# Kernel optimization log

Measured on AMD Instinct MI355X. Metric: run time of the kernel, lower is better.

## Reference

```python
import jax, jax.numpy as jnp
import numpy as np

D_IN = 1024
D_OUT = 1024
N_HEADS = 16
HEAD_DIM = D_OUT // N_HEADS
B = 2
S = 2048


def setup_inputs() -> dict:
    key = jax.random.key(0)
    ks = jax.random.split(key, 6)
    scale = 0.02
    x = jax.random.normal(ks[0], (B, S, D_IN), dtype=jnp.float32)
    # torch nn.Linear stores weight as [out, in]; y = x @ W.T + b
    Wq = jax.random.normal(ks[1], (D_OUT, D_IN), dtype=jnp.float32) * scale
    Wk = jax.random.normal(ks[2], (D_OUT, D_IN), dtype=jnp.float32) * scale
    Wv = jax.random.normal(ks[3], (D_OUT, D_IN), dtype=jnp.float32) * scale
    Wo = jax.random.normal(ks[4], (D_OUT, D_OUT), dtype=jnp.float32) * scale
    bo = jax.random.normal(ks[5], (D_OUT,), dtype=jnp.float32) * scale
    return {"x": x, "Wq": Wq, "Wk": Wk, "Wv": Wv, "Wo": Wo, "bo": bo}


def reference(x, Wq, Wk, Wv, Wo, bo):
    b, n, _ = x.shape
    # projections (no qkv bias)
    q = jnp.einsum('bnd,ed->bne', x, Wq).reshape(b, n, N_HEADS, HEAD_DIM).transpose(0, 2, 1, 3)
    k = jnp.einsum('bnd,ed->bne', x, Wk).reshape(b, n, N_HEADS, HEAD_DIM).transpose(0, 2, 1, 3)
    v = jnp.einsum('bnd,ed->bne', x, Wv).reshape(b, n, N_HEADS, HEAD_DIM).transpose(0, 2, 1, 3)
    # scores [b, h, s, s]
    scores = jnp.einsum('bhqd,bhkd->bhqk', q, k) / jnp.sqrt(jnp.float32(HEAD_DIM))
    causal = jnp.tril(jnp.ones((n, n), dtype=bool))
    scores = jnp.where(causal, scores, -jnp.inf)
    attn = jax.nn.softmax(scores, axis=-1)  # dropout p=0 -> identity
    ctx = jnp.einsum('bhqk,bhkd->bhqd', attn, v)
    ctx = ctx.transpose(0, 2, 1, 3).reshape(b, n, D_OUT)
    out = jnp.einsum('bnd,ed->bne', ctx, Wo) + bo
    return out
```

## Files before the change

### kernel.cpp

```cpp
#include <hip/hip_runtime.h>

typedef unsigned short u16;
typedef unsigned int u32;
typedef short bf16x8 __attribute__((ext_vector_type(8)));
typedef short bf16x4 __attribute__((ext_vector_type(4)));
typedef float f32x4 __attribute__((ext_vector_type(4)));
typedef u32 u32x2 __attribute__((ext_vector_type(2)));

#define LOG2E 1.4426950408889634f
#define QSCALE (0.125f * LOG2E)

__device__ __forceinline__ u16 f2b(float f) {
  u32 u = __builtin_bit_cast(u32, f);
  u32 r = (u + 0x7FFFu + ((u >> 16) & 1u)) >> 16;
  return (u16)r;
}

__device__ __forceinline__ bf16x8 cvt8(const float* p) {
  const f32x4 a = *(const f32x4*)p;
  const f32x4 b = *(const f32x4*)(p + 4);
  bf16x8 r = { (short)f2b(a[0]), (short)f2b(a[1]), (short)f2b(a[2]),
               (short)f2b(a[3]), (short)f2b(b[0]), (short)f2b(b[1]),
               (short)f2b(b[2]), (short)f2b(b[3]) };
  return r;
}

__device__ __forceinline__ void gl_lds16(const u16* g, u16* l) {
  __builtin_amdgcn_global_load_lds(
      (const __attribute__((address_space(1))) u32*)(const void*)g,
      (__attribute__((address_space(3))) u32*)(void*)l, 16, 0, 0);
}

__global__ __launch_bounds__(256) void convert_qw_kernel(
    const float* __restrict__ x, const float* __restrict__ wq,
    const float* __restrict__ wk, const float* __restrict__ wv,
    u16* __restrict__ xb, u16* __restrict__ wb) {
  const int i = blockIdx.x * 256 + threadIdx.x;
  if (i >= 917504) return;
  const float* src;
  u16* dst;
  size_t off;
  if (i < 524288) {
    src = x; dst = xb; off = (size_t)i * 8;
  } else {
    const int j = i - 524288;
    const int mat = j >> 17, r = j & 131071;
    src = (mat == 0) ? wq : ((mat == 1) ? wk : wv);
    dst = wb + (size_t)mat * 1048576u;
    off = (size_t)r * 8;
  }
  *(bf16x8*)(dst + off) = cvt8(src + off);
}

__global__ __launch_bounds__(256) void convert_wo_kernel(
    const float* __restrict__ wo, u16* __restrict__ wob) {
  const int i = blockIdx.x * 256 + threadIdx.x;
  if (i >= 131072) return;
  const size_t off = (size_t)i * 8;
  *(bf16x8*)(wob + off) = cvt8(wo + off);
}

__device__ __forceinline__ void gemm_core2(const u16* A, const u16* W,
                                           int m0, int n0, int tid,
                                           u16* As, u16* Bs,
                                           f32x4 (&acc)[4][4]) {
  const int lane = tid & 63, wave = tid >> 6;
  const int wr = wave >> 1, wc = wave & 1;
  const int l15 = lane & 15, quad = lane >> 4;

  const int srow = wave * 16 + (lane >> 2);
  const int csrc =
      (((lane & 3) ^ ((lane >> 2) & 3) ^ ((lane >> 4) & 3)) << 3);
  const u16* ga = A + (size_t)(m0 + srow) * 1024 + csrc;
  const u16* gw = W + (size_t)(n0 + srow) * 1024 + csrc;
  u16* la = As + wave * 16 * 32;
  u16* lb = Bs + wave * 16 * 32;

  const int rswz = (l15 & 3) ^ ((l15 >> 2) & 3);
  const u16* ar = As + (wr * 64 + l15) * 32 + ((quad ^ rswz) << 3);
  const u16* br = Bs + (wc * 64 + l15) * 32 + ((quad ^ rswz) << 3);

  for (int k0 = 0; k0 < 1024; k0 += 32) {
    __syncthreads();
    gl_lds16(ga + k0, la);
    gl_lds16(ga + k0 + (size_t)64 * 1024, la + 64 * 32);
    gl_lds16(gw + k0, lb);
    gl_lds16(gw + k0 + (size_t)64 * 1024, lb + 64 * 32);
    __syncthreads();
    bf16x8 af[4], bfr[4];
#pragma unroll
    for (int i = 0; i < 4; ++i) af[i] = *(const bf16x8*)(ar + i * 16 * 32);
#pragma unroll
    for (int i = 0; i < 4; ++i) bfr[i] = *(const bf16x8*)(br + i * 16 * 32);
#pragma unroll
    for (int mt = 0; mt < 4; ++mt)
#pragma unroll
      for (int nt = 0; nt < 4; ++nt)
        acc[mt][nt] = __builtin_amdgcn_mfma_f32_16x16x32_bf16(
            af[mt], bfr[nt], acc[mt][nt], 0, 0, 0);
  }
}

__global__ __launch_bounds__(256, 3) void gemm_qkv_kernel(
    const u16* __restrict__ xb, const u16* __restrict__ wb,
    u16* __restrict__ qo, u16* __restrict__ ko, u16* __restrict__ vt) {
  __shared__ __align__(16) u16 As[128 * 32];
  __shared__ __align__(16) u16 Bs[128 * 32];
  const int tid = threadIdx.x;
  const int m0 = blockIdx.x * 128;
  const int mat = blockIdx.y >> 3;
  const int n0 = (blockIdx.y & 7) * 128;
  const u16* W = wb + (size_t)mat * 1048576u;

  f32x4 acc[4][4] = {};
  gemm_core2(xb, W, m0, n0, tid, As, Bs, acc);

  const int lane = tid & 63, wave = tid >> 6;
  const int wr = wave >> 1, wc = wave & 1;
  const int l15 = lane & 15, quad = lane >> 4;

  if (mat < 2) {
    u16* out = (mat == 0) ? qo : ko;
    const float sc = (mat == 0) ? QSCALE : 1.0f;
#pragma unroll
    for (int mt = 0; mt < 4; ++mt) {
      const int gr = m0 + wr * 64 + mt * 16 + quad * 4;
#pragma unroll
      for (int nt = 0; nt < 4; ++nt) {
        const int gc = n0 + wc * 64 + nt * 16 + l15;
#pragma unroll
        for (int r = 0; r < 4; ++r)
          out[(size_t)(gr + r) * 1024 + gc] = f2b(acc[mt][nt][r] * sc);
      }
    }
  } else {
#pragma unroll
    for (int mt = 0; mt < 4; ++mt) {
      const int gr = m0 + wr * 64 + mt * 16 + quad * 4;
      const int b = gr >> 11;
      const int s = gr & 2047;
#pragma unroll
      for (int nt = 0; nt < 4; ++nt) {
        const int gc = n0 + wc * 64 + nt * 16 + l15;
        bf16x4 pk = { (short)f2b(acc[mt][nt][0]), (short)f2b(acc[mt][nt][1]),
                      (short)f2b(acc[mt][nt][2]), (short)f2b(acc[mt][nt][3]) };
        *(bf16x4*)&vt[(size_t)(b * 1024 + gc) * 2048 + s] = pk;
      }
    }
  }
}

__global__ __launch_bounds__(256, 3) void gemm_out_kernel(
    const u16* __restrict__ ctx, const u16* __restrict__ wob,
    const float* __restrict__ bo, float* __restrict__ out) {
  __shared__ __align__(16) u16 As[128 * 32];
  __shared__ __align__(16) u16 Bs[128 * 32];
  const int tid = threadIdx.x;
  const int m0 = blockIdx.x * 128;
  const int n0 = blockIdx.y * 128;

  f32x4 acc[4][4] = {};
  gemm_core2(ctx, wob, m0, n0, tid, As, Bs, acc);

  const int lane = tid & 63, wave = tid >> 6;
  const int wr = wave >> 1, wc = wave & 1;
  const int l15 = lane & 15, quad = lane >> 4;
#pragma unroll
  for (int nt = 0; nt < 4; ++nt) {
    const int gc = n0 + wc * 64 + nt * 16 + l15;
    const float bv = bo[gc];
#pragma unroll
    for (int mt = 0; mt < 4; ++mt) {
      const int gr = m0 + wr * 64 + mt * 16 + quad * 4;
#pragma unroll
      for (int r = 0; r < 4; ++r)
        out[(size_t)(gr + r) * 1024 + gc] = acc[mt][nt][r] + bv;
    }
  }
}

__global__ __launch_bounds__(256, 4) void flash_kernel(
    const u16* q, const u16* __restrict__ k,
    const u16* __restrict__ vt, u16* ctx) {
  __shared__ __align__(16) u16 Ks[2][4096];
  __shared__ __align__(16) u16 Vs[2][4096];
  __shared__ __align__(16) u16 plds_all[4][1024];

  const int tid = threadIdx.x;
  const int wave = tid >> 6, lane = tid & 63;
  const int l15 = lane & 15, quad = lane >> 4;

  const int g = blockIdx.x;
  const int xcd = g & 7;
  const int s = g >> 3;
  const int bh_local = s >> 5;
  const int c = s & 31;
  const int qv = (bh_local & 1) ? (31 - c) : c;
  const int q0b = qv * 64;
  const int ntiles = qv + 1;
  const int bh = xcd + 8 * bh_local;
  const int b = bh >> 4, h = bh & 15;
  const int m = q0b + wave * 16 + l15;

  const u16* qrow = q + ((size_t)(b * 2048 + m) * 1024 + h * 64);
  const bf16x8 qf0 = *(const bf16x8*)(qrow + quad * 8);
  const bf16x8 qf1 = *(const bf16x8*)(qrow + 32 + quad * 8);

  const int sr = wave * 16 + (lane >> 3);
  const int csrc = (((lane & 7) ^ ((lane >> 3) & 7)) << 3);
  const u16* kg = k + (size_t)(b * 2048) * 1024 + h * 64;
  const u16* vg = vt + (size_t)(b * 1024 + h * 64) * 2048;
  u16* plds = plds_all[wave];
  const int swz = (l15 & 7);

  f32x4 o[4] = {};
  float m_run = -INFINITY, l_lane = 0.0f;

#pragma unroll
  for (int i = 0; i < 2; ++i) {
    const int r = sr + i * 8;
    gl_lds16(kg + (size_t)r * 1024 + csrc, &Ks[0][wave * 1024 + i * 512]);
    gl_lds16(vg + (size_t)r * 2048 + csrc, &Vs[0][wave * 1024 + i * 512]);
  }
  __syncthreads();

  int buf = 0;
  for (int t = 0; t < ntiles; ++t) {
    const int n0 = t * 64;
    if (t + 1 < ntiles) {
      const int n1 = n0 + 64;
      const int nb = buf ^ 1;
#pragma unroll
      for (int i = 0; i < 2; ++i) {
        const int r = sr + i * 8;
        gl_lds16(kg + (size_t)(n1 + r) * 1024 + csrc,
                 &Ks[nb][wave * 1024 + i * 512]);
        gl_lds16(vg + (size_t)r * 2048 + n1 + csrc,
                 &Vs[nb][wave * 1024 + i * 512]);
      }
    }

    f32x4 st[4];
#pragma unroll
    for (int s4 = 0; s4 < 4; ++s4) {
      const u16* kr = &Ks[buf][(s4 * 16 + l15) * 64];
      const bf16x8 kf0 = *(const bf16x8*)(kr + ((quad ^ swz) << 3));
      const bf16x8 kf1 = *(const bf16x8*)(kr + (((4 | quad) ^ swz) << 3));
      f32x4 a = {};
      a = __builtin_amdgcn_mfma_f32_16x16x32_bf16(kf0, qf0, a, 0, 0, 0);
      a = __builtin_amdgcn_mfma_f32_16x16x32_bf16(kf1, qf1, a, 0, 0, 0);
      st[s4] = a;
    }

    float s[16];
#pragma unroll
    for (int s4 = 0; s4 < 4; ++s4)
#pragma unroll
      for (int r = 0; r < 4; ++r) s[s4 * 4 + r] = st[s4][r];
    if (t == ntiles - 1) {
#pragma unroll
      for (int s4 = 0; s4 < 4; ++s4)
#pragma unroll
        for (int r = 0; r < 4; ++r) {
          const int kv = n0 + s4 * 16 + quad * 4 + r;
          if (kv > m) s[s4 * 4 + r] = -INFINITY;
        }
    }
    float t8[8], t4[4];
#pragma unroll
    for (int i = 0; i < 8; ++i) t8[i] = fmaxf(s[i], s[i + 8]);
#pragma unroll
    for (int i = 0; i < 4; ++i) t4[i] = fmaxf(t8[i], t8[i + 4]);
    float mx = fmaxf(fmaxf(t4[0], t4[1]), fmaxf(t4[2], t4[3]));
    mx = fmaxf(mx, __shfl_xor(mx, 16));
    mx = fmaxf(mx, __shfl_xor(mx, 32));

    float mbase;
    if (__all(mx <= m_run + 8.0f)) {
      mbase = m_run;
    } else {
      mbase = fmaxf(m_run, mx);
      const float alpha = exp2f(m_run - mbase);
      l_lane *= alpha;
#pragma unroll
      for (int dt = 0; dt < 4; ++dt) o[dt] *= alpha;
      m_run = mbase;
    }

    float p[16];
#pragma unroll
    for (int i = 0; i < 16; ++i) p[i] = exp2f(s[i] - mbase);
    float u8[8], u4[4];
#pragma unroll
    for (int i = 0; i < 8; ++i) u8[i] = p[i] + p[i + 8];
#pragma unroll
    for (int i = 0; i < 4; ++i) u4[i] = u8[i] + u8[i + 4];
    l_lane += (u4[0] + u4[1]) + (u4[2] + u4[3]);

#pragma unroll
    for (int s4 = 0; s4 < 4; ++s4) {
      u32 c0, c1;
      asm("v_cvt_pk_bf16_f32 %0, %1, %2"
          : "=v"(c0) : "v"(p[s4 * 4 + 0]), "v"(p[s4 * 4 + 1]));
      asm("v_cvt_pk_bf16_f32 %0, %1, %2"
          : "=v"(c1) : "v"(p[s4 * 4 + 2]), "v"(p[s4 * 4 + 3]));
      const int wchunk = ((s4 * 2 + (quad >> 1)) ^ swz) << 3;
      u32x2 w = { c0, c1 };
      *(u32x2*)&plds[l15 * 64 + wchunk + ((quad & 1) << 2)] = w;
    }
    asm volatile("s_waitcnt lgkmcnt(0)" ::: "memory");

#pragma unroll
    for (int ks = 0; ks < 2; ++ks) {
      const bf16x8 pf =
          *(const bf16x8*)&plds[l15 * 64 + (((ks * 4 + quad) ^ swz) << 3)];
#pragma unroll
      for (int dt = 0; dt < 4; ++dt) {
        const u16* vr = &Vs[buf][(dt * 16 + l15) * 64];
        const bf16x8 vf =
            *(const bf16x8*)(vr + ((((ks << 2) | quad) ^ swz) << 3));
        o[dt] = __builtin_amdgcn_mfma_f32_16x16x32_bf16(vf, pf, o[dt], 0, 0, 0);
      }
    }

    __syncthreads();
    buf ^= 1;
  }

  float l = l_lane;
  l += __shfl_xor(l, 16);
  l += __shfl_xor(l, 32);
  const float inv = 1.0f / l;
  u16* crow = ctx + ((size_t)(b * 2048 + m) * 1024 + h * 64);
#pragma unroll
  for (int dt = 0; dt < 4; ++dt) {
    bf16x4 ov = { (short)f2b(o[dt][0] * inv), (short)f2b(o[dt][1] * inv),
                  (short)f2b(o[dt][2] * inv), (short)f2b(o[dt][3] * inv) };
    *(bf16x4*)&crow[dt * 16 + quad * 4] = ov;
  }
}

extern "C" void kernel_launch(void* const* d_in, const int* in_sizes, int n_in,
                              void* d_out, int out_size, void* d_ws,
                              size_t ws_size, hipStream_t stream) {
  const float* x  = (const float*)d_in[0];
  const float* wq = (const float*)d_in[1];
  const float* wk = (const float*)d_in[2];
  const float* wv = (const float*)d_in[3];
  const float* wo = (const float*)d_in[4];
  const float* bo = (const float*)d_in[5];
  float* out = (float*)d_out;

  u16* qb = (u16*)d_ws;
  u16* kb = qb + 4194304u;
  u16* vt = kb + 4194304u;
  u16* ctx = qb;

  u16* xb = (u16*)d_out;
  u16* wb = xb + 4194304u;
  u16* wob = kb;

  convert_qw_kernel<<<3584, 256, 0, stream>>>(x, wq, wk, wv, xb, wb);
  gemm_qkv_kernel<<<dim3(32, 24), 256, 0, stream>>>(xb, wb, qb, kb, vt);
  flash_kernel<<<1024, 256, 0, stream>>>(qb, kb, vt, ctx);
  convert_wo_kernel<<<512, 256, 0, stream>>>(wo, wob);
  gemm_out_kernel<<<dim3(32, 8), 256, 0, stream>>>(ctx, wob, bo, out);
}
```

Measured before the change: 191.7 us.

## Double-buffer GEMM LDS tiles and software-pipeline QK of next tile in flash attention

The shared GEMM core now double-buffers the A/B LDS tiles, issuing the next k-slice's global-to-LDS loads before computing on the current one, with one barrier per iteration instead of two. The flash kernel is restructured so the QK^T scores for tile t+1 are computed while the softmax and PV of tile t proceed. V fragments are preloaded into registers so the K/V buffer can be refilled for tile t+2 earlier. Flash launch bounds drop from 4 to 3 blocks per SM to make room for the extra live registers, trading occupancy for overlap.

```diff
diff --git a/kernel.cpp b/kernel.cpp
--- a/kernel.cpp
+++ b/kernel.cpp
@@ -60,7 +60,7 @@
   *(bf16x8*)(wob + off) = cvt8(wo + off);
 }
 
-__device__ __forceinline__ void gemm_core2(const u16* A, const u16* W,
+__device__ __forceinline__ void gemm_core3(const u16* A, const u16* W,
                                            int m0, int n0, int tid,
                                            u16* As, u16* Bs,
                                            f32x4 (&acc)[4][4]) {
@@ -73,20 +73,28 @@
       (((lane & 3) ^ ((lane >> 2) & 3) ^ ((lane >> 4) & 3)) << 3);
   const u16* ga = A + (size_t)(m0 + srow) * 1024 + csrc;
   const u16* gw = W + (size_t)(n0 + srow) * 1024 + csrc;
-  u16* la = As + wave * 16 * 32;
-  u16* lb = Bs + wave * 16 * 32;
+  const int lo = wave * 16 * 32;
 
   const int rswz = (l15 & 3) ^ ((l15 >> 2) & 3);
-  const u16* ar = As + (wr * 64 + l15) * 32 + ((quad ^ rswz) << 3);
-  const u16* br = Bs + (wc * 64 + l15) * 32 + ((quad ^ rswz) << 3);
-
-  for (int k0 = 0; k0 < 1024; k0 += 32) {
-    __syncthreads();
+  const int aoff = (wr * 64 + l15) * 32 + ((quad ^ rswz) << 3);
+  const int boff = (wc * 64 + l15) * 32 + ((quad ^ rswz) << 3);
+
+  auto stage = [&](int k0, int db) {
+    u16* la = As + db * 4096 + lo;
+    u16* lb = Bs + db * 4096 + lo;
     gl_lds16(ga + k0, la);
     gl_lds16(ga + k0 + (size_t)64 * 1024, la + 64 * 32);
     gl_lds16(gw + k0, lb);
     gl_lds16(gw + k0 + (size_t)64 * 1024, lb + 64 * 32);
-    __syncthreads();
+  };
+
+  stage(0, 0);
+  __syncthreads();
+  int db = 0;
+  for (int k0 = 0; k0 < 1024; k0 += 32) {
+    if (k0 + 32 < 1024) stage(k0 + 32, db ^ 1);
+    const u16* ar = As + db * 4096 + aoff;
+    const u16* br = Bs + db * 4096 + boff;
     bf16x8 af[4], bfr[4];
 #pragma unroll
     for (int i = 0; i < 4; ++i) af[i] = *(const bf16x8*)(ar + i * 16 * 32);
@@ -98,14 +106,16 @@
       for (int nt = 0; nt < 4; ++nt)
         acc[mt][nt] = __builtin_amdgcn_mfma_f32_16x16x32_bf16(
             af[mt], bfr[nt], acc[mt][nt], 0, 0, 0);
+    __syncthreads();
+    db ^= 1;
   }
 }
 
 __global__ __launch_bounds__(256, 3) void gemm_qkv_kernel(
     const u16* __restrict__ xb, const u16* __restrict__ wb,
     u16* __restrict__ qo, u16* __restrict__ ko, u16* __restrict__ vt) {
-  __shared__ __align__(16) u16 As[128 * 32];
-  __shared__ __align__(16) u16 Bs[128 * 32];
+  __shared__ __align__(16) u16 As[2 * 128 * 32];
+  __shared__ __align__(16) u16 Bs[2 * 128 * 32];
   const int tid = threadIdx.x;
   const int m0 = blockIdx.x * 128;
   const int mat = blockIdx.y >> 3;
@@ -113,7 +123,7 @@
   const u16* W = wb + (size_t)mat * 1048576u;
 
   f32x4 acc[4][4] = {};
-  gemm_core2(xb, W, m0, n0, tid, As, Bs, acc);
+  gemm_core3(xb, W, m0, n0, tid, As, Bs, acc);
 
   const int lane = tid & 63, wave = tid >> 6;
   const int wr = wave >> 1, wc = wave & 1;
@@ -153,14 +163,14 @@
 __global__ __launch_bounds__(256, 3) void gemm_out_kernel(
     const u16* __restrict__ ctx, const u16* __restrict__ wob,
     const float* __restrict__ bo, float* __restrict__ out) {
-  __shared__ __align__(16) u16 As[128 * 32];
-  __shared__ __align__(16) u16 Bs[128 * 32];
+  __shared__ __align__(16) u16 As[2 * 128 * 32];
+  __shared__ __align__(16) u16 Bs[2 * 128 * 32];
   const int tid = threadIdx.x;
   const int m0 = blockIdx.x * 128;
   const int n0 = blockIdx.y * 128;
 
   f32x4 acc[4][4] = {};
-  gemm_core2(ctx, wob, m0, n0, tid, As, Bs, acc);
+  gemm_core3(ctx, wob, m0, n0, tid, As, Bs, acc);
 
   const int lane = tid & 63, wave = tid >> 6;
   const int wr = wave >> 1, wc = wave & 1;
@@ -179,7 +189,7 @@
   }
 }
 
-__global__ __launch_bounds__(256, 4) void flash_kernel(
+__global__ __launch_bounds__(256, 3) void flash_kernel(
     const u16* q, const u16* __restrict__ k,
     const u16* __restrict__ vt, u16* ctx) {
   __shared__ __align__(16) u16 Ks[2][4096];
@@ -192,9 +202,9 @@
 
   const int g = blockIdx.x;
   const int xcd = g & 7;
-  const int s = g >> 3;
-  const int bh_local = s >> 5;
-  const int c = s & 31;
+  const int sidx = g >> 3;
+  const int bh_local = sidx >> 5;
+  const int c = sidx & 31;
   const int qv = (bh_local & 1) ? (31 - c) : c;
   const int q0b = qv * 64;
   const int ntiles = qv + 1;
@@ -213,44 +223,54 @@
   u16* plds = plds_all[wave];
   const int swz = (l15 & 7);
 
-  f32x4 o[4] = {};
-  float m_run = -INFINITY, l_lane = 0.0f;
-
-#pragma unroll
-  for (int i = 0; i < 2; ++i) {
-    const int r = sr + i * 8;
-    gl_lds16(kg + (size_t)r * 1024 + csrc, &Ks[0][wave * 1024 + i * 512]);
-    gl_lds16(vg + (size_t)r * 2048 + csrc, &Vs[0][wave * 1024 + i * 512]);
-  }
-  __syncthreads();
-
-  int buf = 0;
-  for (int t = 0; t < ntiles; ++t) {
-    const int n0 = t * 64;
-    if (t + 1 < ntiles) {
-      const int n1 = n0 + 64;
-      const int nb = buf ^ 1;
-#pragma unroll
-      for (int i = 0; i < 2; ++i) {
-        const int r = sr + i * 8;
-        gl_lds16(kg + (size_t)(n1 + r) * 1024 + csrc,
-                 &Ks[nb][wave * 1024 + i * 512]);
-        gl_lds16(vg + (size_t)r * 2048 + n1 + csrc,
-                 &Vs[nb][wave * 1024 + i * 512]);
-      }
-    }
-
-    f32x4 st[4];
+  auto stage = [&](int n, int db) {
+#pragma unroll
+    for (int i = 0; i < 2; ++i) {
+      const int r = sr + i * 8;
+      gl_lds16(kg + (size_t)(n * 64 + r) * 1024 + csrc,
+               &Ks[db][wave * 1024 + i * 512]);
+      gl_lds16(vg + (size_t)r * 2048 + n * 64 + csrc,
+               &Vs[db][wave * 1024 + i * 512]);
+    }
+  };
+  auto qk_tile = [&](int db, f32x4 (&dst)[4]) {
 #pragma unroll
     for (int s4 = 0; s4 < 4; ++s4) {
-      const u16* kr = &Ks[buf][(s4 * 16 + l15) * 64];
+      const u16* kr = &Ks[db][(s4 * 16 + l15) * 64];
       const bf16x8 kf0 = *(const bf16x8*)(kr + ((quad ^ swz) << 3));
       const bf16x8 kf1 = *(const bf16x8*)(kr + (((4 | quad) ^ swz) << 3));
       f32x4 a = {};
       a = __builtin_amdgcn_mfma_f32_16x16x32_bf16(kf0, qf0, a, 0, 0, 0);
       a = __builtin_amdgcn_mfma_f32_16x16x32_bf16(kf1, qf1, a, 0, 0, 0);
-      st[s4] = a;
-    }
+      dst[s4] = a;
+    }
+  };
+
+  f32x4 o[4] = {};
+  float m_run = -INFINITY, l_lane = 0.0f;
+
+  stage(0, 0);
+  __syncthreads();
+  f32x4 st[4];
+  qk_tile(0, st);
+  stage(1, 1);
+
+  int buf = 0;
+  for (int t = 0; t < ntiles; ++t) {
+    __syncthreads();
+
+    bf16x8 vf[8];
+#pragma unroll
+    for (int ks = 0; ks < 2; ++ks)
+#pragma unroll
+      for (int dt = 0; dt < 4; ++dt)
+        vf[ks * 4 + dt] = *(const bf16x8*)(&Vs[buf][(dt * 16 + l15) * 64] +
+                                           ((((ks << 2) | quad) ^ swz) << 3));
+    f32x4 stn[4];
+    if (t + 1 < ntiles) qk_tile(buf ^ 1, stn);
+
+    __syncthreads();
+    if (t + 2 < ntiles) stage(t + 2, buf);
 
     float s[16];
 #pragma unroll
@@ -258,6 +278,7 @@
 #pragma unroll
       for (int r = 0; r < 4; ++r) s[s4 * 4 + r] = st[s4][r];
     if (t == ntiles - 1) {
+      const int n0 = t * 64;
 #pragma unroll
       for (int s4 = 0; s4 < 4; ++s4)
 #pragma unroll
@@ -315,15 +336,15 @@
       const bf16x8 pf =
           *(const bf16x8*)&plds[l15 * 64 + (((ks * 4 + quad) ^ swz) << 3)];
 #pragma unroll
-      for (int dt = 0; dt < 4; ++dt) {
-        const u16* vr = &Vs[buf][(dt * 16 + l15) * 64];
-        const bf16x8 vf =
-            *(const bf16x8*)(vr + ((((ks << 2) | quad) ^ swz) << 3));
-        o[dt] = __builtin_amdgcn_mfma_f32_16x16x32_bf16(vf, pf, o[dt], 0, 0, 0);
-      }
-    }
-
-    __syncthreads();
+      for (int dt = 0; dt < 4; ++dt)
+        o[dt] = __builtin_amdgcn_mfma_f32_16x16x32_bf16(vf[ks * 4 + dt], pf,
+                                                        o[dt], 0, 0, 0);
+    }
+
+    if (t + 1 < ntiles) {
+#pragma unroll
+      for (int s4 = 0; s4 < 4; ++s4) st[s4] = stn[s4];
+    }
     buf ^= 1;
   }
 
```

New measurement: 198.1 us. 3.3% more time.

## Double-buffer GEMM LDS tiles, split-K output GEMM with fused Wo conversion

Applied to the files above, without the earlier changes.

The QKV GEMM core now double-buffers its LDS tiles, prefetching the next K slice while MFMAs run on the current one, and drops one barrier per iteration. The output projection reads fp32 Wo directly, converting it to bf16 in registers before the LDS write, which removes the separate Wo convert kernel. It is also split along K into two halves to double the block count. A new merge kernel sums the two partials and the bias, which adds an extra fp32 read/write pass and one more launch.

```diff
diff --git a/kernel.cpp b/kernel.cpp
--- a/kernel.cpp
+++ b/kernel.cpp
@@ -52,15 +52,7 @@
   *(bf16x8*)(dst + off) = cvt8(src + off);
 }
 
-__global__ __launch_bounds__(256) void convert_wo_kernel(
-    const float* __restrict__ wo, u16* __restrict__ wob) {
-  const int i = blockIdx.x * 256 + threadIdx.x;
-  if (i >= 131072) return;
-  const size_t off = (size_t)i * 8;
-  *(bf16x8*)(wob + off) = cvt8(wo + off);
-}
-
-__device__ __forceinline__ void gemm_core2(const u16* A, const u16* W,
+__device__ __forceinline__ void gemm_core3(const u16* A, const u16* W,
                                            int m0, int n0, int tid,
                                            u16* As, u16* Bs,
                                            f32x4 (&acc)[4][4]) {
@@ -73,20 +65,28 @@
       (((lane & 3) ^ ((lane >> 2) & 3) ^ ((lane >> 4) & 3)) << 3);
   const u16* ga = A + (size_t)(m0 + srow) * 1024 + csrc;
   const u16* gw = W + (size_t)(n0 + srow) * 1024 + csrc;
-  u16* la = As + wave * 16 * 32;
-  u16* lb = Bs + wave * 16 * 32;
+  const int lo = wave * 16 * 32;
 
   const int rswz = (l15 & 3) ^ ((l15 >> 2) & 3);
-  const u16* ar = As + (wr * 64 + l15) * 32 + ((quad ^ rswz) << 3);
-  const u16* br = Bs + (wc * 64 + l15) * 32 + ((quad ^ rswz) << 3);
-
-  for (int k0 = 0; k0 < 1024; k0 += 32) {
-    __syncthreads();
+  const int aoff = (wr * 64 + l15) * 32 + ((quad ^ rswz) << 3);
+  const int boff = (wc * 64 + l15) * 32 + ((quad ^ rswz) << 3);
+
+  auto stage = [&](int k0, int db) {
+    u16* la = As + db * 4096 + lo;
+    u16* lb = Bs + db * 4096 + lo;
     gl_lds16(ga + k0, la);
     gl_lds16(ga + k0 + (size_t)64 * 1024, la + 64 * 32);
     gl_lds16(gw + k0, lb);
     gl_lds16(gw + k0 + (size_t)64 * 1024, lb + 64 * 32);
-    __syncthreads();
+  };
+
+  stage(0, 0);
+  __syncthreads();
+  int db = 0;
+  for (int k0 = 0; k0 < 1024; k0 += 32) {
+    if (k0 + 32 < 1024) stage(k0 + 32, db ^ 1);
+    const u16* ar = As + db * 4096 + aoff;
+    const u16* br = Bs + db * 4096 + boff;
     bf16x8 af[4], bfr[4];
 #pragma unroll
     for (int i = 0; i < 4; ++i) af[i] = *(const bf16x8*)(ar + i * 16 * 32);
@@ -98,14 +98,91 @@
       for (int nt = 0; nt < 4; ++nt)
         acc[mt][nt] = __builtin_amdgcn_mfma_f32_16x16x32_bf16(
             af[mt], bfr[nt], acc[mt][nt], 0, 0, 0);
+    __syncthreads();
+    db ^= 1;
+  }
+}
+
+__device__ __forceinline__ void gemm_core_out(const u16* A, const float* Wf,
+                                              int m0, int n0, int klo, int tid,
+                                              u16* As, u16* Bs,
+                                              f32x4 (&acc)[4][4]) {
+  const int lane = tid & 63, wave = tid >> 6;
+  const int wr = wave >> 1, wc = wave & 1;
+  const int l15 = lane & 15, quad = lane >> 4;
+
+  const int srow = wave * 16 + (lane >> 2);
+  const int csrc =
+      (((lane & 3) ^ ((lane >> 2) & 3) ^ ((lane >> 4) & 3)) << 3);
+  const u16* ga = A + (size_t)(m0 + srow) * 1024 + csrc;
+  const float* gw = Wf + (size_t)(n0 + srow) * 1024 + csrc;
+  const int lo = wave * 512;
+
+  const int rswz = (l15 & 3) ^ ((l15 >> 2) & 3);
+  const int aoff = (wr * 64 + l15) * 32 + ((quad ^ rswz) << 3);
+  const int boff = (wc * 64 + l15) * 32 + ((quad ^ rswz) << 3);
+
+  auto stageA = [&](int k0, int db) {
+    u16* la = As + db * 4096 + lo;
+    gl_lds16(ga + k0, la);
+    gl_lds16(ga + k0 + (size_t)64 * 1024, la + 64 * 32);
+  };
+  auto loadW = [&](int k0, f32x4 (&w)[4]) {
+    w[0] = *(const f32x4*)(gw + k0);
+    w[1] = *(const f32x4*)(gw + k0 + 4);
+    w[2] = *(const f32x4*)(gw + k0 + 65536);
+    w[3] = *(const f32x4*)(gw + k0 + 65540);
+  };
+  auto writeW = [&](f32x4 (&w)[4], int db) {
+    u16* lb = Bs + db * 4096 + lo + lane * 8;
+    bf16x8 w0 = { (short)f2b(w[0][0]), (short)f2b(w[0][1]), (short)f2b(w[0][2]),
+                  (short)f2b(w[0][3]), (short)f2b(w[1][0]), (short)f2b(w[1][1]),
+                  (short)f2b(w[1][2]), (short)f2b(w[1][3]) };
+    bf16x8 w1 = { (short)f2b(w[2][0]), (short)f2b(w[2][1]), (short)f2b(w[2][2]),
+                  (short)f2b(w[2][3]), (short)f2b(w[3][0]), (short)f2b(w[3][1]),
+                  (short)f2b(w[3][2]), (short)f2b(w[3][3]) };
+    *(bf16x8*)lb = w0;
+    *(bf16x8*)(lb + 2048) = w1;
+  };
+
+  f32x4 wreg[4];
+  stageA(klo, 0);
+  loadW(klo, wreg);
+  writeW(wreg, 0);
+  __syncthreads();
+  int db = 0;
+  const int kend = klo + 512;
+  for (int k0 = klo; k0 < kend; k0 += 32) {
+    const bool more = (k0 + 32 < kend);
+    f32x4 wnext[4];
+    if (more) {
+      stageA(k0 + 32, db ^ 1);
+      loadW(k0 + 32, wnext);
+    }
+    const u16* ar = As + db * 4096 + aoff;
+    const u16* br = Bs + db * 4096 + boff;
+    bf16x8 af[4], bfr[4];
+#pragma unroll
+    for (int i = 0; i < 4; ++i) af[i] = *(const bf16x8*)(ar + i * 16 * 32);
+#pragma unroll
+    for (int i = 0; i < 4; ++i) bfr[i] = *(const bf16x8*)(br + i * 16 * 32);
+#pragma unroll
+    for (int mt = 0; mt < 4; ++mt)
+#pragma unroll
+      for (int nt = 0; nt < 4; ++nt)
+        acc[mt][nt] = __builtin_amdgcn_mfma_f32_16x16x32_bf16(
+            af[mt], bfr[nt], acc[mt][nt], 0, 0, 0);
+    if (more) writeW(wnext, db ^ 1);
+    __syncthreads();
+    db ^= 1;
   }
 }
 
 __global__ __launch_bounds__(256, 3) void gemm_qkv_kernel(
     const u16* __restrict__ xb, const u16* __restrict__ wb,
     u16* __restrict__ qo, u16* __restrict__ ko, u16* __restrict__ vt) {
-  __shared__ __align__(16) u16 As[128 * 32];
-  __shared__ __align__(16) u16 Bs[128 * 32];
+  __shared__ __align__(16) u16 As[2 * 128 * 32];
+  __shared__ __align__(16) u16 Bs[2 * 128 * 32];
   const int tid = threadIdx.x;
   const int m0 = blockIdx.x * 128;
   const int mat = blockIdx.y >> 3;
@@ -113,7 +190,7 @@
   const u16* W = wb + (size_t)mat * 1048576u;
 
   f32x4 acc[4][4] = {};
-  gemm_core2(xb, W, m0, n0, tid, As, Bs, acc);
+  gemm_core3(xb, W, m0, n0, tid, As, Bs, acc);
 
   const int lane = tid & 63, wave = tid >> 6;
   const int wr = wave >> 1, wc = wave & 1;
@@ -150,33 +227,46 @@
   }
 }
 
-__global__ __launch_bounds__(256, 3) void gemm_out_kernel(
-    const u16* __restrict__ ctx, const u16* __restrict__ wob,
-    const float* __restrict__ bo, float* __restrict__ out) {
-  __shared__ __align__(16) u16 As[128 * 32];
-  __shared__ __align__(16) u16 Bs[128 * 32];
+__global__ __launch_bounds__(256, 2) void gemm_out_kernel(
+    const u16* __restrict__ ctx, const float* __restrict__ wo,
+    float* __restrict__ part, float* __restrict__ out) {
+  __shared__ __align__(16) u16 As[2 * 128 * 32];
+  __shared__ __align__(16) u16 Bs[2 * 128 * 32];
   const int tid = threadIdx.x;
   const int m0 = blockIdx.x * 128;
   const int n0 = blockIdx.y * 128;
+  const int klo = blockIdx.z * 512;
 
   f32x4 acc[4][4] = {};
-  gemm_core2(ctx, wob, m0, n0, tid, As, Bs, acc);
-
+  gemm_core_out(ctx, wo, m0, n0, klo, tid, As, Bs, acc);
+
+  float* dst = (blockIdx.z == 0) ? part : out;
   const int lane = tid & 63, wave = tid >> 6;
   const int wr = wave >> 1, wc = wave & 1;
   const int l15 = lane & 15, quad = lane >> 4;
 #pragma unroll
   for (int nt = 0; nt < 4; ++nt) {
     const int gc = n0 + wc * 64 + nt * 16 + l15;
-    const float bv = bo[gc];
 #pragma unroll
     for (int mt = 0; mt < 4; ++mt) {
       const int gr = m0 + wr * 64 + mt * 16 + quad * 4;
 #pragma unroll
       for (int r = 0; r < 4; ++r)
-        out[(size_t)(gr + r) * 1024 + gc] = acc[mt][nt][r] + bv;
-    }
-  }
+        dst[(size_t)(gr + r) * 1024 + gc] = acc[mt][nt][r];
+    }
+  }
+}
+
+__global__ __launch_bounds__(256) void merge_out_kernel(
+    float* __restrict__ out, const float* __restrict__ part,
+    const float* __restrict__ bo) {
+  const int i = (blockIdx.x * 256 + threadIdx.x) * 4;
+  const f32x4 a = *(const f32x4*)(out + i);
+  const f32x4 p = *(const f32x4*)(part + i);
+  const f32x4 bv = *(const f32x4*)(bo + (i & 1023));
+  f32x4 r = { a[0] + p[0] + bv[0], a[1] + p[1] + bv[1],
+              a[2] + p[2] + bv[2], a[3] + p[3] + bv[3] };
+  *(f32x4*)(out + i) = r;
 }
 
 __global__ __launch_bounds__(256, 4) void flash_kernel(
@@ -355,14 +445,14 @@
   u16* kb = qb + 4194304u;
   u16* vt = kb + 4194304u;
   u16* ctx = qb;
+  float* part = (float*)kb;
 
   u16* xb = (u16*)d_out;
   u16* wb = xb + 4194304u;
-  u16* wob = kb;
 
   convert_qw_kernel<<<3584, 256, 0, stream>>>(x, wq, wk, wv, xb, wb);
   gemm_qkv_kernel<<<dim3(32, 24), 256, 0, stream>>>(xb, wb, qb, kb, vt);
   flash_kernel<<<1024, 256, 0, stream>>>(qb, kb, vt, ctx);
-  convert_wo_kernel<<<512, 256, 0, stream>>>(wo, wob);
-  gemm_out_kernel<<<dim3(32, 8), 256, 0, stream>>>(ctx, wob, bo, out);
-}
+  gemm_out_kernel<<<dim3(32, 8, 2), 256, 0, stream>>>(ctx, wo, part, out);
+  merge_out_kernel<<<4096, 256, 0, stream>>>(out, part, bo);
+}
```

After: 196.6 us. +2.5%, slower.
